# Optimization experiments

Hardware: AMD Instinct MI355X
Metric: run time of the kernel (lower is better)

Reference implementation:

```python
import jax, jax.numpy as jnp
import numpy as np

L = 2          # num_layers
H = 1024       # hidden_size
E = 1024       # embedding_size (== H, required by the feedback matmul)
T = 64         # len(list_desc) decision steps


def setup_inputs() -> dict:
    key = jax.random.key(0)
    ks = jax.random.split(key, 6)
    s = 1.0 / np.sqrt(H)  # keep LSTM gates out of saturation
    return {
        "W_ih": jax.random.normal(ks[0], (L, 4 * H, H), jnp.float32) * s,
        "W_hh": jax.random.normal(ks[1], (L, 4 * H, H), jnp.float32) * s,
        "b_ih": jax.random.normal(ks[2], (L, 4 * H), jnp.float32) * s,
        "b_hh": jax.random.normal(ks[3], (L, 4 * H), jnp.float32) * s,
        "We": jax.random.normal(ks[4], (T, E, H), jnp.float32) * s,
        "be": jax.random.normal(ks[5], (T, E), jnp.float32) * s,
    }


def _lstm_multilayer_step(x, h, c, W_ih, W_hh, b_ih, b_hh):
    # x: [1, E]; h, c: [L, 1, H].  PyTorch gate order: i, f, g, o.
    hs, cs = [], []
    inp = x
    for l in range(L):  # small fixed layer loop
        gates = inp @ W_ih[l].T + b_ih[l] + h[l] @ W_hh[l].T + b_hh[l]  # [1, 4H]
        i, f, g, o = jnp.split(gates, 4, axis=-1)
        c_new = jax.nn.sigmoid(f) * c[l] + jax.nn.sigmoid(i) * jnp.tanh(g)
        h_new = jax.nn.sigmoid(o) * jnp.tanh(c_new)
        hs.append(h_new)
        cs.append(c_new)
        inp = h_new
    return jnp.stack(hs), jnp.stack(cs), inp  # inp = top-layer hidden [1, H]


def reference(W_ih, W_hh, b_ih, b_hh, We, be):
    x0 = jnp.zeros((1, E), jnp.float32)
    h0 = jnp.zeros((L, 1, H), jnp.float32)
    c0 = jnp.zeros((L, 1, H), jnp.float32)

    def step(carry, per_step):
        x, h, c = carry
        We_t, be_t = per_step  # [E, H], [E]
        h, c, top = _lstm_multilayer_step(x, h, c, W_ih, W_hh, b_ih, b_hh)
        logits = top @ We_t.T + be_t            # [1, E]
        decision = jax.nn.softmax(logits, -1)    # [1, E]
        x_next = decision @ We_t                 # [1, H] == [1, E]
        return (x_next, h, c), decision

    _, decisions = jax.lax.scan(step, (x0, h0, c0), (We, be))
    return decisions[:, 0, :]  # [T, E] concatenated decisions
```

## Files before the change

### kernel.cpp

```cpp
#include <hip/hip_runtime.h>

static constexpr int L_ = 2;
static constexpr int H_ = 1024;
static constexpr int E_ = 1024;
static constexpr int T_ = 64;
static constexpr int NB = 256;
static constexpr int BT = 1024;
static constexpr int NSYNC = T_ * 4;
static constexpr int NGRP  = 16;

static constexpr int WS_XV   = 0;
static constexpr int WS_HB   = H_;
static constexpr int WS_LG   = H_ + 2 * L_ * H_;
static constexpr int WS_GRP  = WS_LG + E_;
static constexpr int WS_ROOT = WS_GRP + NSYNC * NGRP * 16;
static constexpr int WS_BC   = WS_ROOT + NSYNC * 16;
static constexpr size_t WS_ZERO_BYTES = (size_t)(WS_BC + NSYNC * 16) * 4;

__device__ __forceinline__ float sigm(float v) { return 1.0f / (1.0f + expf(-v)); }

__device__ __forceinline__ float cload(const float* p) {
  return __hip_atomic_load(p, __ATOMIC_RELAXED, __HIP_MEMORY_SCOPE_AGENT);
}
__device__ __forceinline__ void cstore(float* p, float v) {
  __hip_atomic_store(p, v, __ATOMIC_RELAXED, __HIP_MEMORY_SCOPE_AGENT);
}

__device__ __forceinline__ void gsync(unsigned* wsu, int idx, int b) {
  __syncthreads();
  if (threadIdx.x == 0) {
    unsigned* grp  = wsu + WS_GRP  + (idx * NGRP + (b >> 4)) * 16;
    unsigned* root = wsu + WS_ROOT + idx * 16;
    unsigned* bc   = wsu + WS_BC   + idx * 16;
    if (__hip_atomic_fetch_add(grp, 1u, __ATOMIC_RELAXED, __HIP_MEMORY_SCOPE_AGENT) == 15u) {
      if (__hip_atomic_fetch_add(root, 1u, __ATOMIC_RELAXED, __HIP_MEMORY_SCOPE_AGENT) == 15u)
        __hip_atomic_store(bc, 1u, __ATOMIC_RELAXED, __HIP_MEMORY_SCOPE_AGENT);
    }
    while (__hip_atomic_load(bc, __ATOMIC_RELAXED, __HIP_MEMORY_SCOPE_AGENT) == 0u)
      __builtin_amdgcn_s_sleep(1);
  }
  __syncthreads();
}

__global__ __launch_bounds__(BT, 4) void ctrl_kernel(
    const float* __restrict__ W_ih, const float* __restrict__ W_hh,
    const float* __restrict__ b_ih, const float* __restrict__ b_hh,
    const float* __restrict__ We,   const float* __restrict__ be,
    float* __restrict__ out, float* __restrict__ ws)
{
  const int tid  = threadIdx.x;
  const int b    = blockIdx.x;
  const int lane = tid & 63;
  const int w    = tid >> 6;
  const int wl   = w >> 3;
  const int wq   = (w >> 1) & 3;
  const int wh   = w & 1;

  float*    xv     = ws + WS_XV;
  float*    hbuf   = ws + WS_HB;
  float*    logits = ws + WS_LG;
  unsigned* wsu    = (unsigned*)ws;

  const int cswz = ((b & 7) * 32 + (b >> 3)) * 4;

  __shared__ float  s_x[H_];
  __shared__ float  s_h[H_];
  __shared__ float  s_gd[4][2][4];
  __shared__ float  s_bias[2][4][4];
  __shared__ float  s_c[2][4];
  __shared__ float  s_red[16];
  __shared__ float  s_redm[16];
  __shared__ float  s_reds[16];
  __shared__ float4 s_part4[16];

  if (tid < 32) {
    const int l = tid >> 4, q = (tid >> 2) & 3, u = tid & 3;
    const int j = b * 4 + u;
    s_bias[l][q][u] = b_ih[(size_t)l * 4 * H_ + q * H_ + j]
                    + b_hh[(size_t)l * 4 * H_ + q * H_ + j];
  }
  if (tid < 8) s_c[tid >> 2][tid & 3] = 0.0f;

  float4 wr[4][4];
  {
    const float* Wbase = (wh == 0) ? W_ih : W_hh;
    #pragma unroll
    for (int u = 0; u < 4; ++u) {
      const size_t row = (size_t)wl * 4 * H_ * H_
                       + ((size_t)wq * H_ + (size_t)(b * 4 + u)) * (size_t)H_;
      #pragma unroll
      for (int m = 0; m < 4; ++m)
        wr[u][m] = *(const float4*)&Wbase[row + (size_t)m * 256 + lane * 4];
    }
  }
  #pragma unroll
  for (int u = 0; u < 4; ++u) {
    #pragma unroll
    for (int m = 0; m < 4; ++m)
      asm volatile("" : "+v"(wr[u][m].x), "+v"(wr[u][m].y),
                        "+v"(wr[u][m].z), "+v"(wr[u][m].w));
  }

  for (int t = 0; t < T_; ++t) {
    const int cur = t & 1, nxt = cur ^ 1;
    const float* We_t = We + (size_t)t * E_ * H_;
    const float* be_t = be + (size_t)t * E_;

    const float4 wlog = *(const float4*)&We_t[((size_t)(b * 4 + (tid >> 8))) * H_ + (tid & 255) * 4];
    const float4 wfb  = *(const float4*)&We_t[(size_t)tid * H_ + cswz];

    #pragma unroll
    for (int l = 0; l < L_; ++l) {
      s_x[tid] = (l == 0) ? cload(&xv[tid]) : cload(&hbuf[(size_t)nxt * L_ * H_ + tid]);
      s_h[tid] = cload(&hbuf[(size_t)cur * L_ * H_ + l * H_ + tid]);
      __syncthreads();
      if (wl == l) {
        const float4* vin = (const float4*)((wh == 0) ? s_x : s_h);
        float a0 = 0.f, a1 = 0.f, a2 = 0.f, a3 = 0.f;
        #pragma unroll
        for (int m = 0; m < 4; ++m) {
          const float4 x4 = vin[m * 64 + lane];
          a0 += wr[0][m].x * x4.x + wr[0][m].y * x4.y + wr[0][m].z * x4.z + wr[0][m].w * x4.w;
          a1 += wr[1][m].x * x4.x + wr[1][m].y * x4.y + wr[1][m].z * x4.z + wr[1][m].w * x4.w;
          a2 += wr[2][m].x * x4.x + wr[2][m].y * x4.y + wr[2][m].z * x4.z + wr[2][m].w * x4.w;
          a3 += wr[3][m].x * x4.x + wr[3][m].y * x4.y + wr[3][m].z * x4.z + wr[3][m].w * x4.w;
        }
        #pragma unroll
        for (int off = 32; off; off >>= 1) {
          a0 += __shfl_down(a0, off, 64);
          a1 += __shfl_down(a1, off, 64);
          a2 += __shfl_down(a2, off, 64);
          a3 += __shfl_down(a3, off, 64);
        }
        if (lane == 0) {
          s_gd[wq][wh][0] = a0; s_gd[wq][wh][1] = a1;
          s_gd[wq][wh][2] = a2; s_gd[wq][wh][3] = a3;
        }
      }
      __syncthreads();
      if (tid < 4) {
        const int u = tid;
        const float g0 = s_gd[0][0][u] + s_gd[0][1][u] + s_bias[l][0][u];
        const float g1 = s_gd[1][0][u] + s_gd[1][1][u] + s_bias[l][1][u];
        const float g2 = s_gd[2][0][u] + s_gd[2][1][u] + s_bias[l][2][u];
        const float g3 = s_gd[3][0][u] + s_gd[3][1][u] + s_bias[l][3][u];
        const float cn = sigm(g1) * s_c[l][u] + sigm(g0) * tanhf(g2);
        s_c[l][u] = cn;
        cstore(&hbuf[(size_t)nxt * L_ * H_ + l * H_ + b * 4 + u], sigm(g3) * tanhf(cn));
      }
      gsync(wsu, t * 4 + l, b);
    }

    s_x[tid] = cload(&hbuf[(size_t)nxt * L_ * H_ + H_ + tid]);
    __syncthreads();
    {
      const int rr = tid >> 8;
      const float4 h4 = ((const float4*)s_x)[tid & 255];
      float a = wlog.x * h4.x + wlog.y * h4.y + wlog.z * h4.z + wlog.w * h4.w;
      #pragma unroll
      for (int off = 32; off; off >>= 1) a += __shfl_down(a, off, 64);
      if (lane == 0) s_red[w] = a;
      __syncthreads();
      if ((tid & 255) == 0) {
        const int e = b * 4 + rr;
        cstore(&logits[e], s_red[rr * 4] + s_red[rr * 4 + 1] + s_red[rr * 4 + 2]
                         + s_red[rr * 4 + 3] + be_t[e]);
      }
    }
    gsync(wsu, t * 4 + 2, b);

    {
      s_x[tid] = cload(&logits[tid]);
      __syncthreads();
      const float v = s_x[tid];
      float mm = v;
      #pragma unroll
      for (int off = 32; off; off >>= 1) mm = fmaxf(mm, __shfl_down(mm, off, 64));
      if (lane == 0) s_redm[w] = mm;
      __syncthreads();
      mm = s_redm[0];
      #pragma unroll
      for (int k = 1; k < 16; ++k) mm = fmaxf(mm, s_redm[k]);
      const float ev = expf(v - mm);
      float sv = ev;
      #pragma unroll
      for (int off = 32; off; off >>= 1) sv += __shfl_down(sv, off, 64);
      if (lane == 0) s_reds[w] = sv;
      __syncthreads();
      float ssum = 0.f;
      #pragma unroll
      for (int k = 0; k < 16; ++k) ssum += s_reds[k];
      const float inv = 1.0f / ssum;
      const float d = ev * inv;

      if ((tid >> 2) == b) out[(size_t)t * E_ + tid] = d;

      float4 acc = make_float4(d * wfb.x, d * wfb.y, d * wfb.z, d * wfb.w);
      #pragma unroll
      for (int off = 32; off; off >>= 1) {
        acc.x += __shfl_down(acc.x, off, 64);
        acc.y += __shfl_down(acc.y, off, 64);
        acc.z += __shfl_down(acc.z, off, 64);
        acc.w += __shfl_down(acc.w, off, 64);
      }
      if (lane == 0) s_part4[w] = acc;
      __syncthreads();
      if (tid < 4) {
        float s = 0.f;
        #pragma unroll
        for (int k = 0; k < 16; ++k)
          s += ((const float*)&s_part4[k])[tid];
        cstore(&xv[cswz + tid], s);
      }
    }
    gsync(wsu, t * 4 + 3, b);
  }
}

extern "C" void kernel_launch(void* const* d_in, const int* in_sizes, int n_in,
                              void* d_out, int out_size, void* d_ws, size_t ws_size,
                              hipStream_t stream) {
  const float* W_ih = (const float*)d_in[0];
  const float* W_hh = (const float*)d_in[1];
  const float* b_ih = (const float*)d_in[2];
  const float* b_hh = (const float*)d_in[3];
  const float* We   = (const float*)d_in[4];
  const float* be   = (const float*)d_in[5];
  float* out = (float*)d_out;
  float* ws  = (float*)d_ws;

  (void)hipMemsetAsync(ws, 0, WS_ZERO_BYTES, stream);

  void* args[] = {(void*)&W_ih, (void*)&W_hh, (void*)&b_ih, (void*)&b_hh,
                  (void*)&We,   (void*)&be,   (void*)&out,  (void*)&ws};
  (void)hipLaunchCooperativeKernel((const void*)ctrl_kernel, dim3(NB), dim3(BT),
                                   args, 0, stream);
}
```

Before: 1.135 ms.

## Replace grid barriers with sentinel-polled per-step dataflow buffers and overlap recurrent matvecs

```diff
diff --git a/kernel.cpp b/kernel.cpp
--- a/kernel.cpp
+++ b/kernel.cpp
@@ -6,40 +6,26 @@
 static constexpr int T_ = 64;
 static constexpr int NB = 256;
 static constexpr int BT = 1024;
-static constexpr int NSYNC = T_ * 4;
-static constexpr int NGRP  = 16;
-
-static constexpr int WS_XV   = 0;
-static constexpr int WS_HB   = H_;
-static constexpr int WS_LG   = H_ + 2 * L_ * H_;
-static constexpr int WS_GRP  = WS_LG + E_;
-static constexpr int WS_ROOT = WS_GRP + NSYNC * NGRP * 16;
-static constexpr int WS_BC   = WS_ROOT + NSYNC * 16;
-static constexpr size_t WS_ZERO_BYTES = (size_t)(WS_BC + NSYNC * 16) * 4;
+
+static constexpr int WS_XV = 0;
+static constexpr int WS_H  = WS_XV + (T_ + 1) * H_;
+static constexpr int WS_LG = WS_H + T_ * L_ * H_;
+static constexpr size_t WS_BYTES = (size_t)(WS_LG + T_ * E_) * 4;
+
+static constexpr unsigned SENT = 0xFFFFFFFFu;
 
 __device__ __forceinline__ float sigm(float v) { return 1.0f / (1.0f + expf(-v)); }
 
-__device__ __forceinline__ float cload(const float* p) {
-  return __hip_atomic_load(p, __ATOMIC_RELAXED, __HIP_MEMORY_SCOPE_AGENT);
+__device__ __forceinline__ unsigned cload_u(const float* p) {
+  return __hip_atomic_load((const unsigned*)p, __ATOMIC_RELAXED, __HIP_MEMORY_SCOPE_AGENT);
 }
 __device__ __forceinline__ void cstore(float* p, float v) {
   __hip_atomic_store(p, v, __ATOMIC_RELAXED, __HIP_MEMORY_SCOPE_AGENT);
 }
-
-__device__ __forceinline__ void gsync(unsigned* wsu, int idx, int b) {
-  __syncthreads();
-  if (threadIdx.x == 0) {
-    unsigned* grp  = wsu + WS_GRP  + (idx * NGRP + (b >> 4)) * 16;
-    unsigned* root = wsu + WS_ROOT + idx * 16;
-    unsigned* bc   = wsu + WS_BC   + idx * 16;
-    if (__hip_atomic_fetch_add(grp, 1u, __ATOMIC_RELAXED, __HIP_MEMORY_SCOPE_AGENT) == 15u) {
-      if (__hip_atomic_fetch_add(root, 1u, __ATOMIC_RELAXED, __HIP_MEMORY_SCOPE_AGENT) == 15u)
-        __hip_atomic_store(bc, 1u, __ATOMIC_RELAXED, __HIP_MEMORY_SCOPE_AGENT);
-    }
-    while (__hip_atomic_load(bc, __ATOMIC_RELAXED, __HIP_MEMORY_SCOPE_AGENT) == 0u)
-      __builtin_amdgcn_s_sleep(1);
-  }
-  __syncthreads();
+__device__ __forceinline__ float poll1(const float* p) {
+  unsigned v = cload_u(p);
+  while (v == SENT) { __builtin_amdgcn_s_sleep(1); v = cload_u(p); }
+  return __uint_as_float(v);
 }
 
 __global__ __launch_bounds__(BT, 4) void ctrl_kernel(
@@ -56,16 +42,16 @@
   const int wq   = (w >> 1) & 3;
   const int wh   = w & 1;
 
-  float*    xv     = ws + WS_XV;
-  float*    hbuf   = ws + WS_HB;
-  float*    logits = ws + WS_LG;
-  unsigned* wsu    = (unsigned*)ws;
+  float* xv = ws + WS_XV;
+  float* hh = ws + WS_H;
+  float* lg = ws + WS_LG;
 
   const int cswz = ((b & 7) * 32 + (b >> 3)) * 4;
 
   __shared__ float  s_x[H_];
   __shared__ float  s_h[H_];
-  __shared__ float  s_gd[4][2][4];
+  __shared__ float  s_h1[H_];
+  __shared__ float  s_gd[2][4][2][4];
   __shared__ float  s_bias[2][4][4];
   __shared__ float  s_c[2][4];
   __shared__ float  s_red[16];
@@ -94,64 +80,108 @@
     }
   }
   #pragma unroll
-  for (int u = 0; u < 4; ++u) {
+  for (int u = 0; u < 4; ++u)
     #pragma unroll
     for (int m = 0; m < 4; ++m)
       asm volatile("" : "+v"(wr[u][m].x), "+v"(wr[u][m].y),
                         "+v"(wr[u][m].z), "+v"(wr[u][m].w));
-  }
 
   for (int t = 0; t < T_; ++t) {
-    const int cur = t & 1, nxt = cur ^ 1;
     const float* We_t = We + (size_t)t * E_ * H_;
     const float* be_t = be + (size_t)t * E_;
 
     const float4 wlog = *(const float4*)&We_t[((size_t)(b * 4 + (tid >> 8))) * H_ + (tid & 255) * 4];
     const float4 wfb  = *(const float4*)&We_t[(size_t)tid * H_ + cswz];
 
-    #pragma unroll
-    for (int l = 0; l < L_; ++l) {
-      s_x[tid] = (l == 0) ? cload(&xv[tid]) : cload(&hbuf[(size_t)nxt * L_ * H_ + tid]);
-      s_h[tid] = cload(&hbuf[(size_t)cur * L_ * H_ + l * H_ + tid]);
-      __syncthreads();
-      if (wl == l) {
-        const float4* vin = (const float4*)((wh == 0) ? s_x : s_h);
-        float a0 = 0.f, a1 = 0.f, a2 = 0.f, a3 = 0.f;
-        #pragma unroll
-        for (int m = 0; m < 4; ++m) {
-          const float4 x4 = vin[m * 64 + lane];
-          a0 += wr[0][m].x * x4.x + wr[0][m].y * x4.y + wr[0][m].z * x4.z + wr[0][m].w * x4.w;
-          a1 += wr[1][m].x * x4.x + wr[1][m].y * x4.y + wr[1][m].z * x4.z + wr[1][m].w * x4.w;
-          a2 += wr[2][m].x * x4.x + wr[2][m].y * x4.y + wr[2][m].z * x4.z + wr[2][m].w * x4.w;
-          a3 += wr[3][m].x * x4.x + wr[3][m].y * x4.y + wr[3][m].z * x4.z + wr[3][m].w * x4.w;
-        }
-        #pragma unroll
-        for (int off = 32; off; off >>= 1) {
-          a0 += __shfl_down(a0, off, 64);
-          a1 += __shfl_down(a1, off, 64);
-          a2 += __shfl_down(a2, off, 64);
-          a3 += __shfl_down(a3, off, 64);
-        }
-        if (lane == 0) {
-          s_gd[wq][wh][0] = a0; s_gd[wq][wh][1] = a1;
-          s_gd[wq][wh][2] = a2; s_gd[wq][wh][3] = a3;
-        }
-      }
-      __syncthreads();
-      if (tid < 4) {
-        const int u = tid;
-        const float g0 = s_gd[0][0][u] + s_gd[0][1][u] + s_bias[l][0][u];
-        const float g1 = s_gd[1][0][u] + s_gd[1][1][u] + s_bias[l][1][u];
-        const float g2 = s_gd[2][0][u] + s_gd[2][1][u] + s_bias[l][2][u];
-        const float g3 = s_gd[3][0][u] + s_gd[3][1][u] + s_bias[l][3][u];
-        const float cn = sigm(g1) * s_c[l][u] + sigm(g0) * tanhf(g2);
-        s_c[l][u] = cn;
-        cstore(&hbuf[(size_t)nxt * L_ * H_ + l * H_ + b * 4 + u], sigm(g3) * tanhf(cn));
-      }
-      gsync(wsu, t * 4 + l, b);
-    }
-
-    s_x[tid] = cload(&hbuf[(size_t)nxt * L_ * H_ + H_ + tid]);
+    if (t == 0) {
+      s_x[tid] = 0.0f; s_h[tid] = 0.0f; s_h1[tid] = 0.0f;
+    } else {
+      const float* px = &xv[(size_t)t * H_ + tid];
+      const float* ph = &hh[((size_t)(t - 1) * L_ + 0) * H_ + tid];
+      const float* pk = &hh[((size_t)(t - 1) * L_ + 1) * H_ + tid];
+      unsigned vx = cload_u(px), vh = cload_u(ph), vk = cload_u(pk);
+      while (vx == SENT) { __builtin_amdgcn_s_sleep(1); vx = cload_u(px); }
+      while (vh == SENT) { __builtin_amdgcn_s_sleep(1); vh = cload_u(ph); }
+      while (vk == SENT) { __builtin_amdgcn_s_sleep(1); vk = cload_u(pk); }
+      s_x[tid] = __uint_as_float(vx);
+      s_h[tid] = __uint_as_float(vh);
+      s_h1[tid] = __uint_as_float(vk);
+    }
+    __syncthreads();
+    if (wl == 0 || wh == 1) {
+      const float4* vin = (wl == 0) ? ((wh == 0) ? (const float4*)s_x : (const float4*)s_h)
+                                    : (const float4*)s_h1;
+      float a0 = 0.f, a1 = 0.f, a2 = 0.f, a3 = 0.f;
+      #pragma unroll
+      for (int m = 0; m < 4; ++m) {
+        const float4 x4 = vin[m * 64 + lane];
+        a0 += wr[0][m].x * x4.x + wr[0][m].y * x4.y + wr[0][m].z * x4.z + wr[0][m].w * x4.w;
+        a1 += wr[1][m].x * x4.x + wr[1][m].y * x4.y + wr[1][m].z * x4.z + wr[1][m].w * x4.w;
+        a2 += wr[2][m].x * x4.x + wr[2][m].y * x4.y + wr[2][m].z * x4.z + wr[2][m].w * x4.w;
+        a3 += wr[3][m].x * x4.x + wr[3][m].y * x4.y + wr[3][m].z * x4.z + wr[3][m].w * x4.w;
+      }
+      #pragma unroll
+      for (int off = 32; off; off >>= 1) {
+        a0 += __shfl_down(a0, off, 64);
+        a1 += __shfl_down(a1, off, 64);
+        a2 += __shfl_down(a2, off, 64);
+        a3 += __shfl_down(a3, off, 64);
+      }
+      if (lane == 0) {
+        s_gd[wl][wq][wh][0] = a0; s_gd[wl][wq][wh][1] = a1;
+        s_gd[wl][wq][wh][2] = a2; s_gd[wl][wq][wh][3] = a3;
+      }
+    }
+    __syncthreads();
+    if (tid < 4) {
+      const int u = tid;
+      const float g0 = s_gd[0][0][0][u] + s_gd[0][0][1][u] + s_bias[0][0][u];
+      const float g1 = s_gd[0][1][0][u] + s_gd[0][1][1][u] + s_bias[0][1][u];
+      const float g2 = s_gd[0][2][0][u] + s_gd[0][2][1][u] + s_bias[0][2][u];
+      const float g3 = s_gd[0][3][0][u] + s_gd[0][3][1][u] + s_bias[0][3][u];
+      const float cn = sigm(g1) * s_c[0][u] + sigm(g0) * tanhf(g2);
+      s_c[0][u] = cn;
+      cstore(&hh[((size_t)t * L_ + 0) * H_ + b * 4 + u], sigm(g3) * tanhf(cn));
+    }
+
+    s_x[tid] = poll1(&hh[((size_t)t * L_ + 0) * H_ + tid]);
+    __syncthreads();
+    if (wl == 1 && wh == 0) {
+      const float4* vin = (const float4*)s_x;
+      float a0 = 0.f, a1 = 0.f, a2 = 0.f, a3 = 0.f;
+      #pragma unroll
+      for (int m = 0; m < 4; ++m) {
+        const float4 x4 = vin[m * 64 + lane];
+        a0 += wr[0][m].x * x4.x + wr[0][m].y * x4.y + wr[0][m].z * x4.z + wr[0][m].w * x4.w;
+        a1 += wr[1][m].x * x4.x + wr[1][m].y * x4.y + wr[1][m].z * x4.z + wr[1][m].w * x4.w;
+        a2 += wr[2][m].x * x4.x + wr[2][m].y * x4.y + wr[2][m].z * x4.z + wr[2][m].w * x4.w;
+        a3 += wr[3][m].x * x4.x + wr[3][m].y * x4.y + wr[3][m].z * x4.z + wr[3][m].w * x4.w;
+      }
+      #pragma unroll
+      for (int off = 32; off; off >>= 1) {
+        a0 += __shfl_down(a0, off, 64);
+        a1 += __shfl_down(a1, off, 64);
+        a2 += __shfl_down(a2, off, 64);
+        a3 += __shfl_down(a3, off, 64);
+      }
+      if (lane == 0) {
+        s_gd[1][wq][0][0] = a0; s_gd[1][wq][0][1] = a1;
+        s_gd[1][wq][0][2] = a2; s_gd[1][wq][0][3] = a3;
+      }
+    }
+    __syncthreads();
+    if (tid < 4) {
+      const int u = tid;
+      const float g0 = s_gd[1][0][0][u] + s_gd[1][0][1][u] + s_bias[1][0][u];
+      const float g1 = s_gd[1][1][0][u] + s_gd[1][1][1][u] + s_bias[1][1][u];
+      const float g2 = s_gd[1][2][0][u] + s_gd[1][2][1][u] + s_bias[1][2][u];
+      const float g3 = s_gd[1][3][0][u] + s_gd[1][3][1][u] + s_bias[1][3][u];
+      const float cn = sigm(g1) * s_c[1][u] + sigm(g0) * tanhf(g2);
+      s_c[1][u] = cn;
+      cstore(&hh[((size_t)t * L_ + 1) * H_ + b * 4 + u], sigm(g3) * tanhf(cn));
+    }
+
+    s_x[tid] = poll1(&hh[((size_t)t * L_ + 1) * H_ + tid]);
     __syncthreads();
     {
       const int rr = tid >> 8;
@@ -163,14 +193,14 @@
       __syncthreads();
       if ((tid & 255) == 0) {
         const int e = b * 4 + rr;
-        cstore(&logits[e], s_red[rr * 4] + s_red[rr * 4 + 1] + s_red[rr * 4 + 2]
-                         + s_red[rr * 4 + 3] + be_t[e]);
-      }
-    }
-    gsync(wsu, t * 4 + 2, b);
+        cstore(&lg[(size_t)t * E_ + e],
+               s_red[rr * 4] + s_red[rr * 4 + 1] + s_red[rr * 4 + 2]
+             + s_red[rr * 4 + 3] + be_t[e]);
+      }
+    }
 
     {
-      s_x[tid] = cload(&logits[tid]);
+      s_x[tid] = poll1(&lg[(size_t)t * E_ + tid]);
       __syncthreads();
       const float v = s_x[tid];
       float mm = v;
@@ -210,10 +240,9 @@
         #pragma unroll
         for (int k = 0; k < 16; ++k)
           s += ((const float*)&s_part4[k])[tid];
-        cstore(&xv[cswz + tid], s);
-      }
-    }
-    gsync(wsu, t * 4 + 3, b);
+        cstore(&xv[(size_t)(t + 1) * H_ + cswz + tid], s);
+      }
+    }
   }
 }
 
@@ -229,7 +258,7 @@
   float* out = (float*)d_out;
   float* ws  = (float*)d_ws;
 
-  (void)hipMemsetAsync(ws, 0, WS_ZERO_BYTES, stream);
+  (void)hipMemsetAsync(ws, 0xFF, WS_BYTES, stream);
 
   void* args[] = {(void*)&W_ih, (void*)&W_hh, (void*)&b_ih, (void*)&b_hh,
                   (void*)&We,   (void*)&be,   (void*)&out,  (void*)&ws};
```

After: 1.228 ms. 1.08x slower.
